# Kernel optimization log

Hardware: AMD Instinct MI355X
Metric: run time of the kernel (lower is better)

Reference implementation:

```python
import jax, jax.numpy as jnp
import numpy as np

SCORE_THR = 0.01
IOU_THR = 0.1          # NOTE: original layer hardcodes 0.1 in tf.image.non_max_suppression
MAX_DET = 100
NEG = jnp.float32(-1e30)


def _iou_one_vs_all(box, boxes):
    # box: [4] (y1,x1,y2,x2), boxes: [N,4]
    y1 = jnp.maximum(box[0], boxes[:, 0])
    x1 = jnp.maximum(box[1], boxes[:, 1])
    y2 = jnp.minimum(box[2], boxes[:, 2])
    x2 = jnp.minimum(box[3], boxes[:, 3])
    inter = jnp.maximum(y2 - y1, 0.0) * jnp.maximum(x2 - x1, 0.0)
    a = (box[2] - box[0]) * (box[3] - box[1])
    b = (boxes[:, 2] - boxes[:, 0]) * (boxes[:, 3] - boxes[:, 1])
    return inter / (a + b - inter + 1e-8)


def _nms_keep(boxes, scores):
    # Greedy NMS as a keep-mask over N anchors. Matches tf.image.non_max_suppression
    # restricted to anchors with score > SCORE_THR, up to MAX_DET selections.
    s = jnp.where(scores > SCORE_THR, scores, NEG)
    keep0 = jnp.zeros(s.shape, dtype=bool)

    def step(carry, _):
        s, keep = carry
        i = jnp.argmax(s)
        ok = s[i] > NEG * 0.5
        keep = keep.at[i].set(ok)
        iou = _iou_one_vs_all(boxes[i], boxes)
        s = jnp.where((iou > IOU_THR) & ok, NEG, s)
        s = s.at[i].set(NEG)
        return (s, keep), None

    (_, keep), _ = jax.lax.scan(step, (s, keep0), None, length=MAX_DET)
    return keep


def _filter_image(boxes_i, cls_i):
    # boxes_i: [N,4], cls_i: [N,C]
    C = cls_i.shape[1]
    # class-specific NMS: keep mask per class -> [C, N]
    keep = jax.vmap(lambda s: _nms_keep(boxes_i, s))(cls_i.T)
    keep_flat = keep.T.reshape(-1)          # [N*C], (anchor, class) flat order
    flat = cls_i.reshape(-1)                # [N*C]
    masked = jnp.where(keep_flat, flat, NEG)
    vals, idx = jax.lax.top_k(masked, MAX_DET)
    valid = vals > NEG * 0.5
    anchor = idx // C
    label = idx % C
    scores_out = jnp.where(valid, jnp.take(flat, idx), -1.0)
    boxes_out = jnp.where(valid[:, None], boxes_i[anchor], -1.0)
    labels_out = jnp.where(valid, label, -1).astype(jnp.int32)
    return boxes_out, scores_out, labels_out


def setup_inputs() -> dict:
    key = jax.random.key(0)
    k1, k2, k3 = jax.random.split(key, 3)
    B, N, C = 4, 49104, 90
    yx1 = jax.random.uniform(k1, (B, N, 2), dtype=jnp.float32) * 512.0
    hw = jax.random.uniform(k2, (B, N, 2), dtype=jnp.float32) * 128.0 + 1.0
    boxes = jnp.concatenate([yx1, yx1 + hw], axis=-1)          # [B,N,4] y1x1y2x2
    classification = jax.random.uniform(k3, (B, N, C), dtype=jnp.float32)
    return {"boxes": boxes, "classification": classification}


def reference(boxes, classification):
    return jax.vmap(_filter_image)(boxes, classification)
```

## Files before the change

kernel.cpp:

```cpp
#include <hip/hip_runtime.h>
#include <stdint.h>

typedef unsigned long long u64;

#define B_ 4
#define N_ 49104
#define C_ 90
#define NCLS (B_ * C_)
#define MAXK 100
#define THR 0.01f
#define NB2 2048
#define WIN 256
#define KCAP 1024
#define ACH 128
#define NCH ((N_ + ACH - 1) / ACH)
#define CAPC 32
#define NBIN_M 1280
#define BINBASE 0x3F6E0000u
#define BINSH_M 10
#define T0 0.985f
#define CAPSEL 1024

__device__ __forceinline__ float area_of(float y1, float x1, float y2, float x2) {
#pragma clang fp contract(off)
  return (y2 - y1) * (x2 - x1);
}

#define IOU_MID (26843547.0 / 268435456.0)

__device__ __forceinline__ bool iou_gt(float ay1, float ax1, float ay2, float ax2, float aa,
                                       float by1, float bx1, float by2, float bx2, float ba) {
#pragma clang fp contract(off)
  float y1 = fmaxf(ay1, by1);
  float x1 = fmaxf(ax1, bx1);
  float y2 = fminf(ay2, by2);
  float x2 = fminf(ax2, bx2);
  float inter = fmaxf(y2 - y1, 0.0f) * fmaxf(x2 - x1, 0.0f);
  float denom = aa + ba - inter + 1e-8f;
  return (double)inter >= IOU_MID * (double)denom;
}

__device__ __forceinline__ u64 umax64(u64 a, u64 b) { return a > b ? a : b; }

__device__ __forceinline__ u64 shfl_xor_u64(u64 v, int m) {
  int lo = __shfl_xor((int)(unsigned)v, m);
  int hi = __shfl_xor((int)(unsigned)(v >> 32), m);
  return ((u64)(unsigned)hi << 32) | (u64)(unsigned)lo;
}

__device__ __forceinline__ u64 shfl_u64(u64 v, int src) {
  int lo = __shfl((int)(unsigned)v, src);
  int hi = __shfl((int)(unsigned)(v >> 32), src);
  return ((u64)(unsigned)hi << 32) | (u64)(unsigned)lo;
}

__device__ __forceinline__ int key2bin_m(u64 k) {
  int d = (int)((unsigned)(k >> 32) - BINBASE);
  int bin = d >> BINSH_M;
  if (d < 0) bin = 0;
  if (bin > NBIN_M - 1) bin = NBIN_M - 1;
  return bin;
}

__global__ __launch_bounds__(256) void select_kernel(const float* __restrict__ cls,
                                                     u64* __restrict__ keybuf,
                                                     unsigned* __restrict__ cnt,
                                                     int capsel, float t0) {
  __shared__ u64 ll[C_ * CAPC];
  __shared__ unsigned lcnt[C_];
  __shared__ unsigned base_s[C_];
  int blk = blockIdx.x;
  int b = blk / NCH, ch = blk - b * NCH;
  int a0 = ch * ACH;
  int aEnd = a0 + ACH; if (aEnd > N_) aEnd = N_;
  int e0 = a0 * C_;
  int nelem = (aEnd - a0) * C_;
  int tid = threadIdx.x;

  for (int i = tid; i < C_; i += 256) lcnt[i] = 0u;
  __syncthreads();

  const float4* src4 = (const float4*)(cls + (size_t)b * N_ * C_ + e0);
  int n4 = nelem >> 2;
  for (int i4 = tid; i4 < n4; i4 += 256) {
    float4 v = src4[i4];
#pragma unroll
    for (int j = 0; j < 4; ++j) {
      float s = (&v.x)[j];
      if (s > t0) {
        int e = e0 + i4 * 4 + j;
        unsigned n = (unsigned)e / (unsigned)C_;
        unsigned c = (unsigned)e - n * (unsigned)C_;
        u64 key = ((u64)__float_as_uint(s) << 32) | (u64)(0xFFFFFFFFu - n);
        unsigned pos = atomicAdd(&lcnt[c], 1u);
        if (pos < CAPC) {
          ll[c * CAPC + pos] = key;
        } else {
          unsigned g = (unsigned)(b * C_) + c;
          unsigned gp = atomicAdd(&cnt[g * 16], 1u);
          if (gp < (unsigned)capsel) keybuf[(size_t)g * capsel + gp] = key;
        }
      }
    }
  }
  __syncthreads();

  if (tid < C_) {
    unsigned cc = lcnt[tid]; if (cc > CAPC) cc = CAPC;
    base_s[tid] = atomicAdd(&cnt[(b * C_ + tid) * 16], cc);
  }
  __syncthreads();

  for (int i = tid; i < C_ * CAPC; i += 256) {
    int c = i >> 5, j = i & 31;
    unsigned cc = lcnt[c]; if (cc > CAPC) cc = CAPC;
    if ((unsigned)j < cc) {
      unsigned pos = base_s[c] + (unsigned)j;
      if (pos < (unsigned)capsel)
        keybuf[(size_t)(b * C_ + c) * capsel + pos] = ll[i];
    }
  }
}

__global__ __launch_bounds__(256) void nms_kernel(const float* __restrict__ boxes,
                                                  const float* __restrict__ cls,
                                                  const u64* __restrict__ keybuf,
                                                  const unsigned* __restrict__ cnt,
                                                  unsigned* __restrict__ done,
                                                  int capsel, float t0,
                                                  u64* __restrict__ keepkeys,
                                                  int* __restrict__ nk_arr,
                                                  float* __restrict__ out) {
  int gcls = blockIdx.x;
  int b = gcls / C_, c = gcls - b * C_;
  __shared__ u64 karr[KCAP];
  __shared__ unsigned hist[NB2];
  __shared__ unsigned sfx[NB2];
  __shared__ float4 kb[MAXK];
  __shared__ float ka[MAXK];
  __shared__ unsigned wsum[4];
  __shared__ int sh_cnt[4];
  __shared__ int sh_last, sh_thr;
  __shared__ unsigned sh_cc;
  int tid = threadIdx.x;
  int lane = tid & 63;
  int wid = tid >> 6;

  for (int i = tid; i < MAXK; i += 256) keepkeys[(size_t)gcls * MAXK + i] = 0ull;
  for (int i = tid; i < NB2; i += 256) hist[i] = 0u;
  __syncthreads();

  unsigned Mraw = cnt[gcls * 16];
  bool overflow = (Mraw > (unsigned)KCAP);
  int M = overflow ? 0 : (int)Mraw;

  const u64* src = keybuf + (size_t)gcls * capsel;

  const int PK = KCAP / 256;
  u64 kreg[PK];
#pragma unroll
  for (int q = 0; q < PK; ++q) {
    kreg[q] = 0ull;
    int i = q * 256 + tid;
    if (i < M) {
      kreg[q] = src[i];
      atomicAdd(&hist[(unsigned)(kreg[q] >> 44) & (NB2 - 1)], 1u);
    }
  }
  __syncthreads();

  {
    const int W = NB2 / 256;
    unsigned loc[W];
    unsigned psum = 0;
#pragma unroll
    for (int q = 0; q < W; ++q) {
      psum += hist[NB2 - 1 - (tid * W + q)];
      loc[q] = psum;
    }
    unsigned incl = psum;
#pragma unroll
    for (int s = 1; s < 64; s <<= 1) {
      unsigned v = (unsigned)__shfl_up((int)incl, s);
      if (lane >= s) incl += v;
    }
    if (lane == 63) wsum[wid] = incl;
    __syncthreads();
    unsigned bs = incl - psum;
    for (int w2 = 0; w2 < wid; ++w2) bs += wsum[w2];
#pragma unroll
    for (int q = 0; q < W; ++q)
      sfx[NB2 - 1 - (tid * W + q)] = bs + loc[q];
  }
  __syncthreads();

#pragma unroll
  for (int q = 0; q < PK; ++q) {
    int i = q * 256 + tid;
    if (i < M) {
      u64 k = kreg[q];
      unsigned bin = (unsigned)(k >> 44) & (NB2 - 1);
      unsigned old = atomicSub(&hist[bin], 1u);
      karr[sfx[bin] - old] = k;
    }
  }
  __syncthreads();

  {
    u64 mk2[PK]; int mt[PK];
#pragma unroll
    for (int q = 0; q < PK; ++q) {
      mk2[q] = 0ull; mt[q] = -1;
      int i = q * 256 + tid;
      if (i < M) {
        u64 k = karr[i];
        int bin = (int)((unsigned)(k >> 44) & (NB2 - 1));
        int hi2 = (int)sfx[bin];
        int lo2 = (bin == NB2 - 1) ? 0 : (int)sfx[bin + 1];
        int r = lo2;
        for (int j = lo2; j < hi2; ++j) r += (karr[j] > k);
        mk2[q] = k; mt[q] = r;
      }
    }
    __syncthreads();
#pragma unroll
    for (int q = 0; q < PK; ++q)
      if (mt[q] >= 0) karr[mt[q]] = mk2[q];
  }
  __syncthreads();

  const float4* bx4 = (const float4*)(boxes + (size_t)b * N_ * 4);

  int seen = 0;
  int nwin = (M + WIN - 1) / WIN;
  for (int w = 0; w < nwin && seen < MAXK; ++w) {
    int base = w * WIN;
    int ci = base + tid;
    bool have = ci < M;
    u64 myk = 0ull;
    float4 cb = make_float4(0.f, 0.f, 0.f, 0.f);
    float ca = 0.f;
    if (have) {
      myk = karr[ci];
      cb = bx4[0xFFFFFFFFu - (unsigned)(myk & 0xFFFFFFFFull)];
      ca = area_of(cb.x, cb.y, cb.z, cb.w);
    }
    bool dead = !have;
    for (int j = 0; j < seen; ++j) {
      float4 sb = kb[j]; float sa = ka[j];
      dead |= iou_gt(sb.x, sb.y, sb.z, sb.w, sa,
                     cb.x, cb.y, cb.z, cb.w, ca);
    }
    u64 alive = __ballot(!dead);

    int nslice = (((M - base) < WIN ? (M - base) : WIN) + 63) >> 6;
    for (int s = 0; s < nslice; ++s) {
      if (wid == s) {
        int nkl = seen;
        while (alive != 0ull && nkl < MAXK) {
          int bit = __ffsll((long long)alive) - 1;
          u64 rest = alive & (alive - 1ull);
          int nbit = __ffsll((long long)rest) - 1;
          int pidx = nbit >= 0 ? nbit : bit;
          float b1y1 = __shfl(cb.x, bit), b1x1 = __shfl(cb.y, bit);
          float b1y2 = __shfl(cb.z, bit), b1x2 = __shfl(cb.w, bit);
          float a1 = __shfl(ca, bit);
          float b2y1 = __shfl(cb.x, pidx), b2x1 = __shfl(cb.y, pidx);
          float b2y2 = __shfl(cb.z, pidx), b2x2 = __shfl(cb.w, pidx);
          float a2 = __shfl(ca, pidx);
          u64 k1 = shfl_u64(myk, bit);
          u64 k2 = shfl_u64(myk, pidx);
          bool kill1 = iou_gt(b1y1, b1x1, b1y2, b1x2, a1,
                              cb.x, cb.y, cb.z, cb.w, ca);
          bool kill2 = iou_gt(b2y1, b2x1, b2y2, b2x2, a2,
                              cb.x, cb.y, cb.z, cb.w, ca);
          u64 m1 = __ballot(kill1);
          if (lane == 0) {
            unsigned anchor = 0xFFFFFFFFu - (unsigned)(k1 & 0xFFFFFFFFull);
            unsigned flat = anchor * C_ + (unsigned)c;
            keepkeys[(size_t)gcls * MAXK + nkl] =
                (k1 & 0xFFFFFFFF00000000ull) | (u64)(0xFFFFFFFFu - flat);
            kb[nkl] = make_float4(b1y1, b1x1, b1y2, b1x2);
            ka[nkl] = a1;
          }
          ++nkl;
          alive = rest & ~m1;
          if (alive == 0ull || nkl >= MAXK) break;
          if ((__ffsll((long long)alive) - 1) == nbit) {
            u64 m2 = __ballot(kill2);
            if (lane == 0) {
              unsigned anchor = 0xFFFFFFFFu - (unsigned)(k2 & 0xFFFFFFFFull);
              unsigned flat = anchor * C_ + (unsigned)c;
              keepkeys[(size_t)gcls * MAXK + nkl] =
                  (k2 & 0xFFFFFFFF00000000ull) | (u64)(0xFFFFFFFFu - flat);
              kb[nkl] = make_float4(b2y1, b2x1, b2y2, b2x2);
              ka[nkl] = a2;
            }
            ++nkl;
            alive &= ~m2;
          }
        }
        if (lane == 0) sh_cnt[s] = nkl;
      }
      __syncthreads();
      int nkNew = sh_cnt[s];
      if (nkNew >= MAXK) { seen = nkNew; break; }
      if (wid > s && nkNew > seen) {
        bool d2 = false;
        for (int j = seen; j < nkNew; ++j) {
          float4 sb = kb[j]; float sa = ka[j];
          d2 |= iou_gt(sb.x, sb.y, sb.z, sb.w, sa,
                       cb.x, cb.y, cb.z, cb.w, ca);
        }
        alive &= __ballot(!d2);
      }
      seen = nkNew;
    }
  }

  int nkF = seen;
  if (nkF < MAXK) {
    float teff = overflow ? 2.0f : t0;
    const float* sbase = cls + (size_t)b * N_ * C_ + c;
    const float* bx = boxes + (size_t)b * N_ * 4;
    u64* kkp = keepkeys + (size_t)gcls * MAXK;
    u64* red = karr;
    int nk2 = nkF;
    while (nk2 < MAXK) {
      u64 best = 0ull;
      for (int n = tid; n < N_; n += 256) {
        float s = sbase[(size_t)n * C_];
        if (s > THR && s <= teff) {
          float y1 = bx[(size_t)n * 4 + 0], x1 = bx[(size_t)n * 4 + 1];
          float y2 = bx[(size_t)n * 4 + 2], x2 = bx[(size_t)n * 4 + 3];
          float ar = area_of(y1, x1, y2, x2);
          bool ov = false;
          for (int j = 0; j < nk2; ++j) {
            float4 kbj = kb[j];
            if (iou_gt(kbj.x, kbj.y, kbj.z, kbj.w, ka[j], y1, x1, y2, x2, ar)) { ov = true; break; }
          }
          if (!ov) {
            u64 key = ((u64)__float_as_uint(s) << 32) | (u64)(0xFFFFFFFFu - (unsigned)n);
            best = umax64(best, key);
          }
        }
      }
      red[tid] = best;
      __syncthreads();
      for (int sft = 128; sft > 0; sft >>= 1) {
        if (tid < sft) red[tid] = umax64(red[tid], red[tid + sft]);
        __syncthreads();
      }
      u64 sel = red[0];
      __syncthreads();
      if (sel == 0ull) {
        if (tid == 0) {
          unsigned target2 = 0xFFFFFFFFu - (unsigned)c;
          for (int j = 0; j < nk2; ++j)
            if ((unsigned)(kkp[j] & 0xFFFFFFFFull) == target2) kkp[j] = 0ull;
        }
        break;
      }
      unsigned anchor = 0xFFFFFFFFu - (unsigned)(sel & 0xFFFFFFFFull);
      if (tid == 0) {
        float y1 = bx[(size_t)anchor * 4 + 0], x1 = bx[(size_t)anchor * 4 + 1];
        float y2 = bx[(size_t)anchor * 4 + 2], x2 = bx[(size_t)anchor * 4 + 3];
        kb[nk2] = make_float4(y1, x1, y2, x2);
        ka[nk2] = area_of(y1, x1, y2, x2);
        unsigned flat = anchor * C_ + (unsigned)c;
        kkp[nk2] = (sel & 0xFFFFFFFF00000000ull) | (u64)(0xFFFFFFFFu - flat);
      }
      ++nk2;
      __syncthreads();
    }
    nkF = nk2;
  }
  if (tid == 0) nk_arr[gcls] = nkF;

  __syncthreads();
  if (tid == 0) {
    __threadfence();
    sh_last = (atomicAdd(&done[b], 1u) == (unsigned)(C_ - 1)) ? 1 : 0;
  }
  __syncthreads();
  if (!sh_last) return;
  __threadfence();

  {
    const u64* kk = keepkeys + (size_t)b * C_ * MAXK;
    const int TOT = C_ * MAXK;
    unsigned* histm = hist;
    unsigned* sfxm = sfx;
    u64* mk = karr;
    u64* selk = karr + 512;

    for (int i = tid; i < NBIN_M; i += 256) histm[i] = 0u;
    if (tid == 0) { sh_thr = -1; sh_cc = 0u; }
    __syncthreads();
    for (int i = tid; i < TOT; i += 256) {
      u64 k = kk[i];
      if (k != 0ull) atomicAdd(&histm[key2bin_m(k)], 1u);
    }
    __syncthreads();

    const int W = 5;
    int j0 = tid * W;
    unsigned psum = 0;
#pragma unroll
    for (int q = 0; q < W; ++q) {
      int bin = NBIN_M - 1 - (j0 + q);
      if (bin >= 0) psum += histm[bin];
    }
    unsigned incl = psum;
#pragma unroll
    for (int s = 1; s < 64; s <<= 1) {
      unsigned v = (unsigned)__shfl_up((int)incl, s);
      if (lane >= s) incl += v;
    }
    if (lane == 63) wsum[wid] = incl;
    __syncthreads();
    unsigned base = 0;
    for (int w2 = 0; w2 < wid; ++w2) base += wsum[w2];
    unsigned running = base + incl - psum;
    int mythr = -1;
#pragma unroll
    for (int q = 0; q < W; ++q) {
      int bin = NBIN_M - 1 - (j0 + q);
      if (bin >= 0) {
        running += histm[bin];
        sfxm[bin] = running;
        if (mythr < 0 && running >= (unsigned)MAXK) mythr = bin;
      }
    }
    if (mythr >= 0) atomicMax(&sh_thr, mythr);
    __syncthreads();

    int thr = sh_thr; if (thr < 0) thr = 0;
    unsigned S = sfxm[thr];

    if (S <= 512u) {
      for (int i = tid; i < TOT; i += 256) {
        u64 k = kk[i];
        if (k != 0ull && key2bin_m(k) >= thr) {
          unsigned pos = atomicAdd(&sh_cc, 1u);
          mk[pos] = k;
        }
      }
      __syncthreads();
      for (int i = (int)S + tid; i < 512; i += 256) mk[i] = 0ull;
      __syncthreads();
      for (int k2 = 2; k2 <= 512; k2 <<= 1) {
        for (int j = k2 >> 1; j > 0; j >>= 1) {
          int i1 = 2 * tid - (tid & (j - 1));
          int i2 = i1 | j;
          u64 a = mk[i1], bb2 = mk[i2];
          bool desc = ((i1 & k2) == 0);
          bool sw = desc ? (a < bb2) : (a > bb2);
          if (sw) { mk[i1] = bb2; mk[i2] = a; }
          __syncthreads();
        }
      }
      for (int r = tid; r < MAXK; r += 256) selk[r] = mk[r];
      __syncthreads();
    } else {
      if (wid == 0) {
        int c0 = lane, c1 = lane + 64;
        int len0 = (c0 < C_) ? nk_arr[b * C_ + c0] : 0;
        int len1 = (c1 < C_) ? nk_arr[b * C_ + c1] : 0;
        int h0 = 0, h1 = 0;
        auto fetchc = [&](int cc, int& h, int len) -> u64 {
          while (h < len) {
            u64 k = kk[(size_t)cc * MAXK + h];
            if (k != 0ull) return k;
            ++h;
          }
          return 0ull;
        };
        u64 cand0 = (c0 < C_) ? fetchc(c0, h0, len0) : 0ull;
        u64 cand1 = (c1 < C_) ? fetchc(c1, h1, len1) : 0ull;
        for (int r = 0; r < MAXK; ++r) {
          u64 my = umax64(cand0, cand1);
          u64 g = my;
#pragma unroll
          for (int m = 1; m < 64; m <<= 1) g = umax64(g, shfl_xor_u64(g, m));
          if (lane == 0) selk[r] = g;
          if (g != 0ull && my == g) {
            if (cand0 == g) { ++h0; cand0 = fetchc(c0, h0, len0); }
            else            { ++h1; cand1 = fetchc(c1, h1, len1); }
          }
        }
      }
      __syncthreads();
    }

    for (int r = tid; r < MAXK; r += 256) {
      u64 s = selk[r];
      float oy1, ox1, oy2, ox2, sc, lb;
      if (s != 0ull) {
        unsigned flat = 0xFFFFFFFFu - (unsigned)(s & 0xFFFFFFFFull);
        unsigned anchor = flat / C_;
        unsigned label = flat - anchor * C_;
        sc = __uint_as_float((unsigned)(s >> 32));
        const float4 bp = ((const float4*)(boxes + (size_t)b * N_ * 4))[anchor];
        oy1 = bp.x; ox1 = bp.y; oy2 = bp.z; ox2 = bp.w;
        lb = (float)label;
      } else {
        oy1 = ox1 = oy2 = ox2 = -1.0f; sc = -1.0f; lb = -1.0f;
      }
      float* bo = out + ((size_t)b * MAXK + r) * 4;
      bo[0] = oy1; bo[1] = ox1; bo[2] = oy2; bo[3] = ox2;
      out[(size_t)B_ * MAXK * 4 + b * MAXK + r] = sc;
      out[(size_t)B_ * MAXK * 4 + B_ * MAXK + b * MAXK + r] = lb;
    }
  }
}

extern "C" void kernel_launch(void* const* d_in, const int* in_sizes, int n_in,
                              void* d_out, int out_size, void* d_ws, size_t ws_size,
                              hipStream_t stream) {
  const float* boxes = (const float*)d_in[0];
  const float* cls = (const float*)d_in[1];
  char* ws = (char*)d_ws;

  unsigned* cnt = (unsigned*)ws;
  unsigned* done = (unsigned*)(ws + 23040);
  u64* keybuf = (u64*)(ws + 23104);
  size_t off = 23104 + (size_t)NCLS * CAPSEL * 8;
  u64* keepkeys = (u64*)(ws + off);      off += 288000;
  int* nk_arr = (int*)(ws + off);

  hipMemsetAsync(ws, 0, 23104, stream);
  select_kernel<<<B_ * NCH, 256, 0, stream>>>(cls, keybuf, cnt, CAPSEL, T0);
  nms_kernel<<<NCLS, 256, 0, stream>>>(boxes, cls, keybuf, cnt, done, CAPSEL, T0,
                                       keepkeys, nk_arr, (float*)d_out);
}
```

Measured before the change: 185.9 us.

## Widen NMS candidate window with workspace-sized capacity and 512-thread blocks

Raises the per-class candidate capacity (KCAP to 4096, WIN to 512) and picks capsel and the score cutoff t0 at runtime from the available workspace size. A lower t0 admits more pre-selected candidates, so the window-based NMS is less likely to fall back to the slow full-anchor rescan loop. The NMS kernel now runs 512 threads per block, with scan, reduction and bitonic sort adjusted to match. The cost is a larger shared-memory footprint and more keys to sort per class, plus possible lower occupancy.

```diff
diff --git a/kernel.cpp b/kernel.cpp
--- a/kernel.cpp
+++ b/kernel.cpp
@@ -10,16 +10,14 @@
 #define MAXK 100
 #define THR 0.01f
 #define NB2 2048
-#define WIN 256
-#define KCAP 1024
+#define WIN 512
+#define KCAP 4096
 #define ACH 128
 #define NCH ((N_ + ACH - 1) / ACH)
 #define CAPC 32
 #define NBIN_M 1280
 #define BINBASE 0x3F6E0000u
 #define BINSH_M 10
-#define T0 0.985f
-#define CAPSEL 1024
 
 __device__ __forceinline__ float area_of(float y1, float x1, float y2, float x2) {
 #pragma clang fp contract(off)
@@ -122,7 +120,7 @@
   }
 }
 
-__global__ __launch_bounds__(256) void nms_kernel(const float* __restrict__ boxes,
+__global__ __launch_bounds__(512) void nms_kernel(const float* __restrict__ boxes,
                                                   const float* __restrict__ cls,
                                                   const u64* __restrict__ keybuf,
                                                   const unsigned* __restrict__ cnt,
@@ -138,30 +136,30 @@
   __shared__ unsigned sfx[NB2];
   __shared__ float4 kb[MAXK];
   __shared__ float ka[MAXK];
-  __shared__ unsigned wsum[4];
-  __shared__ int sh_cnt[4];
+  __shared__ unsigned wsum[8];
+  __shared__ int sh_cnt[8];
   __shared__ int sh_last, sh_thr;
   __shared__ unsigned sh_cc;
   int tid = threadIdx.x;
   int lane = tid & 63;
   int wid = tid >> 6;
 
-  for (int i = tid; i < MAXK; i += 256) keepkeys[(size_t)gcls * MAXK + i] = 0ull;
-  for (int i = tid; i < NB2; i += 256) hist[i] = 0u;
+  for (int i = tid; i < MAXK; i += 512) keepkeys[(size_t)gcls * MAXK + i] = 0ull;
+  for (int i = tid; i < NB2; i += 512) hist[i] = 0u;
   __syncthreads();
 
   unsigned Mraw = cnt[gcls * 16];
-  bool overflow = (Mraw > (unsigned)KCAP);
+  bool overflow = (Mraw > (unsigned)capsel);
   int M = overflow ? 0 : (int)Mraw;
 
   const u64* src = keybuf + (size_t)gcls * capsel;
 
-  const int PK = KCAP / 256;
+  const int PK = KCAP / 512;
   u64 kreg[PK];
 #pragma unroll
   for (int q = 0; q < PK; ++q) {
     kreg[q] = 0ull;
-    int i = q * 256 + tid;
+    int i = q * 512 + tid;
     if (i < M) {
       kreg[q] = src[i];
       atomicAdd(&hist[(unsigned)(kreg[q] >> 44) & (NB2 - 1)], 1u);
@@ -170,7 +168,7 @@
   __syncthreads();
 
   {
-    const int W = NB2 / 256;
+    const int W = NB2 / 512;
     unsigned loc[W];
     unsigned psum = 0;
 #pragma unroll
@@ -196,7 +194,7 @@
 
 #pragma unroll
   for (int q = 0; q < PK; ++q) {
-    int i = q * 256 + tid;
+    int i = q * 512 + tid;
     if (i < M) {
       u64 k = kreg[q];
       unsigned bin = (unsigned)(k >> 44) & (NB2 - 1);
@@ -211,7 +209,7 @@
 #pragma unroll
     for (int q = 0; q < PK; ++q) {
       mk2[q] = 0ull; mt[q] = -1;
-      int i = q * 256 + tid;
+      int i = q * 512 + tid;
       if (i < M) {
         u64 k = karr[i];
         int bin = (int)((unsigned)(k >> 44) & (NB2 - 1));
@@ -328,7 +326,7 @@
     int nk2 = nkF;
     while (nk2 < MAXK) {
       u64 best = 0ull;
-      for (int n = tid; n < N_; n += 256) {
+      for (int n = tid; n < N_; n += 512) {
         float s = sbase[(size_t)n * C_];
         if (s > THR && s <= teff) {
           float y1 = bx[(size_t)n * 4 + 0], x1 = bx[(size_t)n * 4 + 1];
@@ -347,7 +345,7 @@
       }
       red[tid] = best;
       __syncthreads();
-      for (int sft = 128; sft > 0; sft >>= 1) {
+      for (int sft = 256; sft > 0; sft >>= 1) {
         if (tid < sft) red[tid] = umax64(red[tid], red[tid + sft]);
         __syncthreads();
       }
@@ -394,20 +392,20 @@
     u64* mk = karr;
     u64* selk = karr + 512;
 
-    for (int i = tid; i < NBIN_M; i += 256) histm[i] = 0u;
+    for (int i = tid; i < NBIN_M; i += 512) histm[i] = 0u;
     if (tid == 0) { sh_thr = -1; sh_cc = 0u; }
     __syncthreads();
-    for (int i = tid; i < TOT; i += 256) {
+    for (int i = tid; i < TOT; i += 512) {
       u64 k = kk[i];
       if (k != 0ull) atomicAdd(&histm[key2bin_m(k)], 1u);
     }
     __syncthreads();
 
-    const int W = 5;
-    int j0 = tid * W;
+    const int Wm = 3;
+    int j0 = tid * Wm;
     unsigned psum = 0;
 #pragma unroll
-    for (int q = 0; q < W; ++q) {
+    for (int q = 0; q < Wm; ++q) {
       int bin = NBIN_M - 1 - (j0 + q);
       if (bin >= 0) psum += histm[bin];
     }
@@ -419,12 +417,12 @@
     }
     if (lane == 63) wsum[wid] = incl;
     __syncthreads();
-    unsigned base = 0;
+    unsigned base = incl - psum;
     for (int w2 = 0; w2 < wid; ++w2) base += wsum[w2];
-    unsigned running = base + incl - psum;
+    unsigned running = base;
     int mythr = -1;
 #pragma unroll
-    for (int q = 0; q < W; ++q) {
+    for (int q = 0; q < Wm; ++q) {
       int bin = NBIN_M - 1 - (j0 + q);
       if (bin >= 0) {
         running += histm[bin];
@@ -439,7 +437,7 @@
     unsigned S = sfxm[thr];
 
     if (S <= 512u) {
-      for (int i = tid; i < TOT; i += 256) {
+      for (int i = tid; i < TOT; i += 512) {
         u64 k = kk[i];
         if (k != 0ull && key2bin_m(k) >= thr) {
           unsigned pos = atomicAdd(&sh_cc, 1u);
@@ -447,20 +445,22 @@
         }
       }
       __syncthreads();
-      for (int i = (int)S + tid; i < 512; i += 256) mk[i] = 0ull;
+      for (int i = (int)S + tid; i < 512; i += 512) mk[i] = 0ull;
       __syncthreads();
       for (int k2 = 2; k2 <= 512; k2 <<= 1) {
         for (int j = k2 >> 1; j > 0; j >>= 1) {
-          int i1 = 2 * tid - (tid & (j - 1));
-          int i2 = i1 | j;
-          u64 a = mk[i1], bb2 = mk[i2];
-          bool desc = ((i1 & k2) == 0);
-          bool sw = desc ? (a < bb2) : (a > bb2);
-          if (sw) { mk[i1] = bb2; mk[i2] = a; }
+          if (tid < 256) {
+            int i1 = 2 * tid - (tid & (j - 1));
+            int i2 = i1 | j;
+            u64 a = mk[i1], bb2 = mk[i2];
+            bool desc = ((i1 & k2) == 0);
+            bool sw = desc ? (a < bb2) : (a > bb2);
+            if (sw) { mk[i1] = bb2; mk[i2] = a; }
+          }
           __syncthreads();
         }
       }
-      for (int r = tid; r < MAXK; r += 256) selk[r] = mk[r];
+      for (int r = tid; r < MAXK; r += 512) selk[r] = mk[r];
       __syncthreads();
     } else {
       if (wid == 0) {
@@ -493,7 +493,7 @@
       __syncthreads();
     }
 
-    for (int r = tid; r < MAXK; r += 256) {
+    for (int r = tid; r < MAXK; r += 512) {
       u64 s = selk[r];
       float oy1, ox1, oy2, ox2, sc, lb;
       if (s != 0ull) {
@@ -522,15 +522,23 @@
   const float* cls = (const float*)d_in[1];
   char* ws = (char*)d_ws;
 
+  int capsel; float t0;
+  auto need_for = [](int cap) -> size_t {
+    return 23104 + (size_t)NCLS * cap * 8 + 288000 + 1440;
+  };
+  if (ws_size >= need_for(4096))      { capsel = 4096; t0 = 0.93f;  }
+  else if (ws_size >= need_for(2048)) { capsel = 2048; t0 = 0.962f; }
+  else                                { capsel = 1024; t0 = 0.985f; }
+
   unsigned* cnt = (unsigned*)ws;
   unsigned* done = (unsigned*)(ws + 23040);
   u64* keybuf = (u64*)(ws + 23104);
-  size_t off = 23104 + (size_t)NCLS * CAPSEL * 8;
+  size_t off = 23104 + (size_t)NCLS * capsel * 8;
   u64* keepkeys = (u64*)(ws + off);      off += 288000;
   int* nk_arr = (int*)(ws + off);
 
   hipMemsetAsync(ws, 0, 23104, stream);
-  select_kernel<<<B_ * NCH, 256, 0, stream>>>(cls, keybuf, cnt, CAPSEL, T0);
-  nms_kernel<<<NCLS, 256, 0, stream>>>(boxes, cls, keybuf, cnt, done, CAPSEL, T0,
+  select_kernel<<<B_ * NCH, 256, 0, stream>>>(cls, keybuf, cnt, capsel, t0);
+  nms_kernel<<<NCLS, 512, 0, stream>>>(boxes, cls, keybuf, cnt, done, capsel, t0,
                                        keepkeys, nk_arr, (float*)d_out);
 }
```

New measurement: 193.1 us. +3.8%, slower.
